# Kernel tuning notes

Hardware: AMD Instinct MI355X
Metric: run time of the kernel (lower is better)

## Reference

```python
import jax, jax.numpy as jnp
import numpy as np

N = 50000   # nodes
E = 800000  # edges (avg degree 16)
D = 128     # in_dim == hidden_dim


def setup_inputs() -> dict:
    key = jax.random.key(0)
    ks = jax.random.split(key, 8)
    x = jax.random.normal(ks[0], (N, D), dtype=jnp.float32)
    edge_index = jax.random.randint(ks[1], (2, E), 0, N, dtype=jnp.int32)
    s = 1.0 / np.sqrt(D)  # glorot-ish scale
    W0 = jax.random.normal(ks[2], (D, D), dtype=jnp.float32) * s
    W1 = jax.random.normal(ks[3], (D, D), dtype=jnp.float32) * s
    W2 = jax.random.normal(ks[4], (D, D), dtype=jnp.float32) * s
    b0 = jnp.zeros((D,), dtype=jnp.float32)
    b1 = jnp.zeros((D,), dtype=jnp.float32)
    b2 = jnp.zeros((D,), dtype=jnp.float32)
    return {"x": x, "edge_index": edge_index,
            "W0": W0, "b0": b0, "W1": W1, "b1": b1, "W2": W2, "b2": b2}


def reference(x, edge_index, W0, b0, W1, b1, W2, b2):
    # PyG GCNConv defaults: add self-loops, symmetric D^-1/2 (A+I) D^-1/2 norm,
    # linear transform first, bias added after aggregation.
    src, dst = edge_index[0], edge_index[1]
    loops = jnp.arange(N, dtype=src.dtype)
    src_f = jnp.concatenate([src, loops])  # [E+N]
    dst_f = jnp.concatenate([dst, loops])
    deg = jax.ops.segment_sum(jnp.ones_like(src_f, dtype=x.dtype), dst_f, num_segments=N)
    dinv = jnp.where(deg > 0, jax.lax.rsqrt(deg), 0.0)
    norm = dinv[src_f] * dinv[dst_f]  # [E+N]

    def gcn_layer(h, W, b):
        h = h @ W                                # [N, D]
        msg = h[src_f] * norm[:, None]           # [E+N, D] gather
        agg = jax.ops.segment_sum(msg, dst_f, num_segments=N)  # scatter-add
        return agg + b

    h = jax.nn.relu(gcn_layer(x, W0, b0))  # dropout p=0.0 is a no-op
    h = jax.nn.relu(gcn_layer(h, W1, b1))
    return gcn_layer(h, W2, b2)
```

## Files before the change

kernel.cpp:

```cpp
#include <hip/hip_runtime.h>
#include <hip/hip_fp16.h>

#define NN 50000
#define NPAD 50048
#define NE 800000
#define D 128
#define BPAD 136

typedef __attribute__((ext_vector_type(8))) short bf16x8;
typedef __attribute__((ext_vector_type(4))) float f32x4;

__device__ inline unsigned short f2bf(float f) {
    unsigned int b = __float_as_uint(f);
    return (unsigned short)((b + 0x7FFFu + ((b >> 16) & 1u)) >> 16);
}
__device__ inline float bf2f(unsigned short u) {
    return __uint_as_float(((unsigned int)u) << 16);
}


__global__ void k_degree(const int* __restrict__ dst, int* __restrict__ cnt,
                         int* __restrict__ rank) {
    int e = blockIdx.x * 256 + threadIdx.x;
    if (e < NE) {
        int d = dst[e];
        int r = atomicAdd(&cnt[d], 1);
        __builtin_nontemporal_store(r, &rank[e]);
    }
}

__global__ void k_scan_block(const int* __restrict__ cnt, int* __restrict__ excl,
                             int* __restrict__ bsum) {
    __shared__ int sm[256];
    int t = threadIdx.x;
    int idx = blockIdx.x * 256 + t;
    int v = (idx < NN) ? cnt[idx] : 0;
    sm[t] = v;
    __syncthreads();
    for (int o = 1; o < 256; o <<= 1) {
        int u = (t >= o) ? sm[t - o] : 0;
        __syncthreads();
        sm[t] += u;
        __syncthreads();
    }
    if (idx < NN) excl[idx] = sm[t] - v;
    if (t == 255) bsum[blockIdx.x] = sm[255];
}

__global__ void k_scan_top(const int* __restrict__ bsum, int* __restrict__ boff) {
    __shared__ int sm[256];
    const int NB = (NN + 255) / 256;
    int t = threadIdx.x;
    int v = (t < NB) ? bsum[t] : 0;
    sm[t] = v;
    __syncthreads();
    for (int o = 1; o < 256; o <<= 1) {
        int u = (t >= o) ? sm[t - o] : 0;
        __syncthreads();
        sm[t] += u;
        __syncthreads();
    }
    if (t < NB) boff[t] = sm[t] - v;
}

__global__ void k_scan_add(int* __restrict__ rowptr, const int* __restrict__ boff,
                           const int* __restrict__ cnt, float* __restrict__ dinv) {
    int idx = blockIdx.x * 256 + threadIdx.x;
    if (idx < NN) {
        rowptr[idx] += boff[idx >> 8];
        dinv[idx] = rsqrtf((float)(cnt[idx] + 1));
    } else if (idx == NN) {
        rowptr[NN] = NE;
    }
}

__global__ void k_fill(const int* __restrict__ src, const int* __restrict__ dst,
                       const int* __restrict__ rowptr, const int* __restrict__ rank,
                       int* __restrict__ col) {
    int e = blockIdx.x * 256 + threadIdx.x;
    if (e < NE) {
        int d = dst[e];
        int pos = rowptr[d] + rank[e];
        __builtin_nontemporal_store(src[e], &col[pos]);
    }
}


__global__ void k_convW3(const float* __restrict__ W0, const float* __restrict__ W1,
                         const float* __restrict__ W2, unsigned short* __restrict__ Wh,
                         unsigned short* __restrict__ Wl) {
    int i = blockIdx.x * 256 + threadIdx.x;
    if (i >= 3 * D * D) return;
    int m = i / (D * D), r = i - m * (D * D);
    const float* W = (m == 0) ? W0 : ((m == 1) ? W1 : W2);
    int k = r >> 7, c = r & 127;
    float v = W[r];
    unsigned short h = f2bf(v);
    unsigned short l = f2bf(v - bf2f(h));
    Wh[(size_t)m * D * D + c * D + k] = h;
    Wl[(size_t)m * D * D + c * D + k] = l;
}


__device__ inline void gemm_store(f32x4 acc[2][4], const float* __restrict__ dinv,
                                  __half* __restrict__ C, int R0, int C0, int lr, int lg) {
    #pragma unroll
    for (int fr = 0; fr < 2; fr++) {
        int rb = R0 + fr * 16 + lg * 4;
        #pragma unroll
        for (int j = 0; j < 4; j++) {
            int r = rb + j;
            if (r < NN) {
                float s = dinv[r];
                #pragma unroll
                for (int fc = 0; fc < 4; fc++)
                    C[(size_t)r * D + C0 + fc * 16 + lr] =
                        __float2half_rn(acc[fr][fc][j] * s);
            }
        }
    }
}


__global__ __launch_bounds__(256, 2) void k_gemm_mfma_x(
        const float* __restrict__ X,
        const unsigned short* __restrict__ BhT, const unsigned short* __restrict__ BlT,
        const float* __restrict__ dinv, __half* __restrict__ C) {
    __shared__ short Bs_h[D * BPAD];
    int t = threadIdx.x;
    {
        int c = t >> 1;
        int k0 = (t & 1) * 64;
        const unsigned short* gh = BhT + c * D + k0;
        short* dh = Bs_h + c * BPAD + k0;
        #pragma unroll
        for (int i = 0; i < 8; i++)
            *(int4*)(dh + i * 8) = *(const int4*)(gh + i * 8);
    }
    __syncthreads();

    int w = t >> 6, ln = t & 63;
    int wr = w >> 1, wc = w & 1;
    int R0 = blockIdx.x * 64 + wr * 32;
    int C0 = wc * 64;
    int lr = ln & 15, lg = ln >> 4;

    f32x4 acc[2][4];
    #pragma unroll
    for (int a = 0; a < 2; a++)
        #pragma unroll
        for (int b = 0; b < 4; b++)
            acc[a][b] = (f32x4){0.f, 0.f, 0.f, 0.f};

    const float* Ab = X + (size_t)(R0 + lr) * D + lg * 8;

    #pragma unroll
    for (int ks = 0; ks < 4; ks++) {
        int ko = ks * 32;
        bf16x8 fa_h[2], fa_l[2], fb_h[4], fb_l[4];
        #pragma unroll
        for (int fr = 0; fr < 2; fr++) {
            float4 p0 = *(const float4*)(Ab + fr * 16 * D + ko);
            float4 p1 = *(const float4*)(Ab + fr * 16 * D + ko + 4);
            float vv[8] = {p0.x, p0.y, p0.z, p0.w, p1.x, p1.y, p1.z, p1.w};
            #pragma unroll
            for (int j = 0; j < 8; j++) {
                unsigned short h = f2bf(vv[j]);
                fa_h[fr][j] = (short)h;
                fa_l[fr][j] = (short)f2bf(vv[j] - bf2f(h));
            }
        }
        #pragma unroll
        for (int fc = 0; fc < 4; fc++) {
            int ccol = C0 + fc * 16 + lr;
            fb_h[fc] = *(const bf16x8*)(Bs_h + ccol * BPAD + ko + lg * 8);
            fb_l[fc] = *(const bf16x8*)(BlT + (size_t)ccol * D + ko + lg * 8);
        }
        #pragma unroll
        for (int fr = 0; fr < 2; fr++) {
            #pragma unroll
            for (int fc = 0; fc < 4; fc++) {
                acc[fr][fc] = __builtin_amdgcn_mfma_f32_16x16x32_bf16(
                    fa_h[fr], fb_h[fc], acc[fr][fc], 0, 0, 0);
                acc[fr][fc] = __builtin_amdgcn_mfma_f32_16x16x32_bf16(
                    fa_l[fr], fb_h[fc], acc[fr][fc], 0, 0, 0);
                acc[fr][fc] = __builtin_amdgcn_mfma_f32_16x16x32_bf16(
                    fa_h[fr], fb_l[fc], acc[fr][fc], 0, 0, 0);
            }
        }
    }
    gemm_store(acc, dinv, C, R0, C0, lr, lg);
}


__global__ __launch_bounds__(256, 3) void k_gemm_mfma_h(
        const __half* __restrict__ H,
        const unsigned short* __restrict__ BhT, const unsigned short* __restrict__ BlT,
        const float* __restrict__ dinv, __half* __restrict__ C) {
    __shared__ short Bs_h[D * BPAD];
    int t = threadIdx.x;
    {
        int c = t >> 1;
        int k0 = (t & 1) * 64;
        const unsigned short* gh = BhT + c * D + k0;
        short* dh = Bs_h + c * BPAD + k0;
        #pragma unroll
        for (int i = 0; i < 8; i++)
            *(int4*)(dh + i * 8) = *(const int4*)(gh + i * 8);
    }
    __syncthreads();

    int w = t >> 6, ln = t & 63;
    int wr = w >> 1, wc = w & 1;
    int R0 = blockIdx.x * 64 + wr * 32;
    int C0 = wc * 64;
    int lr = ln & 15, lg = ln >> 4;

    f32x4 acc[2][4];
    #pragma unroll
    for (int a = 0; a < 2; a++)
        #pragma unroll
        for (int b = 0; b < 4; b++)
            acc[a][b] = (f32x4){0.f, 0.f, 0.f, 0.f};

    const __half* Ab = H + (size_t)(R0 + lr) * D + lg * 8;

    #pragma unroll
    for (int ks = 0; ks < 4; ks++) {
        int ko = ks * 32;
        bf16x8 fa_h[2], fa_l[2], fb_h[4], fb_l[4];
        #pragma unroll
        for (int fr = 0; fr < 2; fr++) {
            float4 p = *(const float4*)(Ab + fr * 16 * D + ko);
            const __half2* hp = (const __half2*)&p;
            #pragma unroll
            for (int q = 0; q < 4; q++) {
                float2 fv = __half22float2(hp[q]);
                unsigned short h0 = f2bf(fv.x), h1 = f2bf(fv.y);
                fa_h[fr][q * 2]     = (short)h0;
                fa_h[fr][q * 2 + 1] = (short)h1;
                fa_l[fr][q * 2]     = (short)f2bf(fv.x - bf2f(h0));
                fa_l[fr][q * 2 + 1] = (short)f2bf(fv.y - bf2f(h1));
            }
        }
        #pragma unroll
        for (int fc = 0; fc < 4; fc++) {
            int ccol = C0 + fc * 16 + lr;
            fb_h[fc] = *(const bf16x8*)(Bs_h + ccol * BPAD + ko + lg * 8);
            fb_l[fc] = *(const bf16x8*)(BlT + (size_t)ccol * D + ko + lg * 8);
        }
        #pragma unroll
        for (int fr = 0; fr < 2; fr++) {
            #pragma unroll
            for (int fc = 0; fc < 4; fc++) {
                acc[fr][fc] = __builtin_amdgcn_mfma_f32_16x16x32_bf16(
                    fa_h[fr], fb_h[fc], acc[fr][fc], 0, 0, 0);
                acc[fr][fc] = __builtin_amdgcn_mfma_f32_16x16x32_bf16(
                    fa_l[fr], fb_h[fc], acc[fr][fc], 0, 0, 0);
                acc[fr][fc] = __builtin_amdgcn_mfma_f32_16x16x32_bf16(
                    fa_h[fr], fb_l[fc], acc[fr][fc], 0, 0, 0);
            }
        }
    }
    gemm_store(acc, dinv, C, R0, C0, lr, lg);
}


__global__ __launch_bounds__(256) void k_agg_relu(const __half* __restrict__ T,
                                                  const int* __restrict__ rowptr,
                                                  const int* __restrict__ col,
                                                  const float* __restrict__ dinv,
                                                  const float* __restrict__ bias,
                                                  __half* __restrict__ Hout) {
    int i = blockIdx.x * 16 + (threadIdx.x >> 4);
    int sl = threadIdx.x & 15;
    int f = sl * 8;
    float di = dinv[i];
    float a[8];
    {
        float4 raw = *(const float4*)(T + (size_t)i * D + f);
        const __half2* hp = (const __half2*)&raw;
        #pragma unroll
        for (int q = 0; q < 4; q++) {
            float2 fv = __half22float2(hp[q]);
            a[q * 2] = fv.x;
            a[q * 2 + 1] = fv.y;
        }
    }
    int e = rowptr[i], r1 = rowptr[i + 1];
    for (; e + 8 <= r1; e += 8) {
        float4 rv[8];
        #pragma unroll
        for (int u = 0; u < 8; u++) {
            int s = col[e + u];
            rv[u] = *(const float4*)(T + (size_t)s * D + f);
        }
        #pragma unroll
        for (int u = 0; u < 8; u++) {
            const __half2* hp = (const __half2*)&rv[u];
            #pragma unroll
            for (int q = 0; q < 4; q++) {
                float2 fv = __half22float2(hp[q]);
                a[q * 2] += fv.x;
                a[q * 2 + 1] += fv.y;
            }
        }
    }
    for (; e < r1; e++) {
        int s = col[e];
        float4 rv = *(const float4*)(T + (size_t)s * D + f);
        const __half2* hp = (const __half2*)&rv;
        #pragma unroll
        for (int q = 0; q < 4; q++) {
            float2 fv = __half22float2(hp[q]);
            a[q * 2] += fv.x;
            a[q * 2 + 1] += fv.y;
        }
    }
    float4 bv0 = *(const float4*)(bias + f);
    float4 bv1 = *(const float4*)(bias + f + 4);
    float bb[8] = {bv0.x, bv0.y, bv0.z, bv0.w, bv1.x, bv1.y, bv1.z, bv1.w};
    __half2 o[4];
    #pragma unroll
    for (int q = 0; q < 4; q++) {
        float x0 = fmaxf(a[q * 2] * di + bb[q * 2], 0.f);
        float x1 = fmaxf(a[q * 2 + 1] * di + bb[q * 2 + 1], 0.f);
        o[q] = __floats2half2_rn(x0, x1);
    }
    *(float4*)(Hout + (size_t)i * D + f) = *(float4*)o;
}

__global__ __launch_bounds__(256) void k_agg_out(const __half* __restrict__ T,
                                                 const int* __restrict__ rowptr,
                                                 const int* __restrict__ col,
                                                 const float* __restrict__ dinv,
                                                 const float* __restrict__ bias,
                                                 float* __restrict__ Of) {
    int i = blockIdx.x * 16 + (threadIdx.x >> 4);
    int sl = threadIdx.x & 15;
    int f = sl * 8;
    float di = dinv[i];
    float a[8];
    {
        float4 raw = *(const float4*)(T + (size_t)i * D + f);
        const __half2* hp = (const __half2*)&raw;
        #pragma unroll
        for (int q = 0; q < 4; q++) {
            float2 fv = __half22float2(hp[q]);
            a[q * 2] = fv.x;
            a[q * 2 + 1] = fv.y;
        }
    }
    int e = rowptr[i], r1 = rowptr[i + 1];
    for (; e + 8 <= r1; e += 8) {
        float4 rv[8];
        #pragma unroll
        for (int u = 0; u < 8; u++) {
            int s = col[e + u];
            rv[u] = *(const float4*)(T + (size_t)s * D + f);
        }
        #pragma unroll
        for (int u = 0; u < 8; u++) {
            const __half2* hp = (const __half2*)&rv[u];
            #pragma unroll
            for (int q = 0; q < 4; q++) {
                float2 fv = __half22float2(hp[q]);
                a[q * 2] += fv.x;
                a[q * 2 + 1] += fv.y;
            }
        }
    }
    for (; e < r1; e++) {
        int s = col[e];
        float4 rv = *(const float4*)(T + (size_t)s * D + f);
        const __half2* hp = (const __half2*)&rv;
        #pragma unroll
        for (int q = 0; q < 4; q++) {
            float2 fv = __half22float2(hp[q]);
            a[q * 2] += fv.x;
            a[q * 2 + 1] += fv.y;
        }
    }
    float4 bv0 = *(const float4*)(bias + f);
    float4 bv1 = *(const float4*)(bias + f + 4);
    float4 o0 = make_float4(a[0] * di + bv0.x, a[1] * di + bv0.y,
                            a[2] * di + bv0.z, a[3] * di + bv0.w);
    float4 o1 = make_float4(a[4] * di + bv1.x, a[5] * di + bv1.y,
                            a[6] * di + bv1.z, a[7] * di + bv1.w);
    *(float4*)(Of + (size_t)i * D + f) = o0;
    *(float4*)(Of + (size_t)i * D + f + 4) = o1;
}


extern "C" void kernel_launch(void* const* d_in, const int* in_sizes, int n_in,
                              void* d_out, int out_size, void* d_ws, size_t ws_size,
                              hipStream_t stream) {
    const float* x  = (const float*)d_in[0];
    const int* edge = (const int*)d_in[1];
    const float* W0 = (const float*)d_in[2];
    const float* b0 = (const float*)d_in[3];
    const float* W1 = (const float*)d_in[4];
    const float* b1 = (const float*)d_in[5];
    const float* W2 = (const float*)d_in[6];
    const float* b2 = (const float*)d_in[7];
    const int* src = edge;
    const int* dst = edge + NE;
    float* out = (float*)d_out;

    char* ws = (char*)d_ws;
    size_t off = 0;
    auto alloc = [&](size_t bytes) {
        void* p = ws + off;
        off += (bytes + 255) & ~(size_t)255;
        return p;
    };
    int*   cnt    = (int*)alloc(NN * 4);
    int*   rowptr = (int*)alloc((NN + 1) * 4);
    float* dinv   = (float*)alloc(NN * 4);
    int*   bsum   = (int*)alloc(256 * 4);
    int*   boff   = (int*)alloc(256 * 4);
    int*   rank   = (int*)alloc((size_t)NE * 4);
    int*   col    = (int*)alloc((size_t)NE * 4);
    unsigned short* Wh = (unsigned short*)alloc(3 * D * D * 2);
    unsigned short* Wl = (unsigned short*)alloc(3 * D * D * 2);
    __half* Ta = (__half*)alloc((size_t)NPAD * D * 2);
    __half* Tb = (__half*)alloc((size_t)NPAD * D * 2);
    __half* Hb = (__half*)alloc((size_t)NPAD * D * 2);

    hipMemsetAsync(cnt, 0, NN * 4, stream);

    k_degree<<<(NE + 255) / 256, 256, 0, stream>>>(dst, cnt, rank);
    k_scan_block<<<(NN + 255) / 256, 256, 0, stream>>>(cnt, rowptr, bsum);
    k_scan_top<<<1, 256, 0, stream>>>(bsum, boff);
    k_scan_add<<<(NN + 256) / 256, 256, 0, stream>>>(rowptr, boff, cnt, dinv);
    k_fill<<<(NE + 255) / 256, 256, 0, stream>>>(src, dst, rowptr, rank, col);
    k_convW3<<<(3 * D * D + 255) / 256, 256, 0, stream>>>(W0, W1, W2, Wh, Wl);

    const int ggrid = (NN + 63) / 64;
    const int agrid = NN / 16;

    k_gemm_mfma_x<<<ggrid, 256, 0, stream>>>(x, Wh, Wl, dinv, Ta);
    k_agg_relu<<<agrid, 256, 0, stream>>>(Ta, rowptr, col, dinv, b0, Hb);
    k_gemm_mfma_h<<<ggrid, 256, 0, stream>>>(Hb, Wh + D * D, Wl + D * D, dinv, Tb);
    k_agg_relu<<<agrid, 256, 0, stream>>>(Tb, rowptr, col, dinv, b1, Hb);
    k_gemm_mfma_h<<<ggrid, 256, 0, stream>>>(Hb, Wh + 2 * D * D, Wl + 2 * D * D, dinv, Ta);
    k_agg_out<<<agrid, 256, 0, stream>>>(Ta, rowptr, col, dinv, b2, out);
}
```

Measured before the change: 243.6 us.

## Fuse setup kernels and load edge indices cooperatively via wave shuffles

Merges the weight bf16-split conversion into the degree-count kernel and folds the top-level scan into the block-scan kernel using a last-block ticket counter, which cuts the number of kernel launches. The aggregation kernels now load eight column indices with one coalesced load per group of lanes and broadcast them with shuffles, instead of each lane loading them all. Edges are processed in masked batches of eight with no scalar tail loop, so tail iterations issue some redundant gathers. This adds an extra memset for the counter and relies on a threadfence-based handoff between blocks.

Measured after the change: 238.5 us. 1.02x faster.

```diff
diff --git a/kernel.cpp b/kernel.cpp
--- a/kernel.cpp
+++ b/kernel.cpp
@@ -6,6 +6,8 @@
 #define NE 800000
 #define D 128
 #define BPAD 136
+#define EGRID 3125
+#define NB 196
 
 typedef __attribute__((ext_vector_type(8))) short bf16x8;
 typedef __attribute__((ext_vector_type(4))) float f32x4;
@@ -19,19 +21,39 @@
 }
 
 
-__global__ void k_degree(const int* __restrict__ dst, int* __restrict__ cnt,
-                         int* __restrict__ rank) {
-    int e = blockIdx.x * 256 + threadIdx.x;
-    if (e < NE) {
-        int d = dst[e];
-        int r = atomicAdd(&cnt[d], 1);
-        __builtin_nontemporal_store(r, &rank[e]);
+__global__ void k_degree_convW(const int* __restrict__ dst, int* __restrict__ cnt,
+                               int* __restrict__ rank,
+                               const float* __restrict__ W0, const float* __restrict__ W1,
+                               const float* __restrict__ W2,
+                               unsigned short* __restrict__ Wh, unsigned short* __restrict__ Wl) {
+    int bid = blockIdx.x;
+    int t = threadIdx.x;
+    if (bid < EGRID) {
+        int e = bid * 256 + t;
+        if (e < NE) {
+            int d = dst[e];
+            int r = atomicAdd(&cnt[d], 1);
+            __builtin_nontemporal_store(r, &rank[e]);
+        }
+    } else {
+        int i = (bid - EGRID) * 256 + t;
+        if (i >= 3 * D * D) return;
+        int m = i / (D * D), r = i - m * (D * D);
+        const float* W = (m == 0) ? W0 : ((m == 1) ? W1 : W2);
+        int k = r >> 7, c = r & 127;
+        float v = W[r];
+        unsigned short h = f2bf(v);
+        unsigned short l = f2bf(v - bf2f(h));
+        Wh[(size_t)m * D * D + c * D + k] = h;
+        Wl[(size_t)m * D * D + c * D + k] = l;
     }
 }
 
 __global__ void k_scan_block(const int* __restrict__ cnt, int* __restrict__ excl,
-                             int* __restrict__ bsum) {
+                             int* __restrict__ bsum, int* __restrict__ boff,
+                             int* __restrict__ counter) {
     __shared__ int sm[256];
+    __shared__ int lastflag;
     int t = threadIdx.x;
     int idx = blockIdx.x * 256 + t;
     int v = (idx < NN) ? cnt[idx] : 0;
@@ -45,14 +67,16 @@
     }
     if (idx < NN) excl[idx] = sm[t] - v;
     if (t == 255) bsum[blockIdx.x] = sm[255];
-}
-
-__global__ void k_scan_top(const int* __restrict__ bsum, int* __restrict__ boff) {
-    __shared__ int sm[256];
-    const int NB = (NN + 255) / 256;
-    int t = threadIdx.x;
-    int v = (t < NB) ? bsum[t] : 0;
-    sm[t] = v;
+    __threadfence();
+    if (t == 0) {
+        int ticket = atomicAdd(counter, 1);
+        lastflag = (ticket == NB - 1);
+    }
+    __syncthreads();
+    if (!lastflag) return;
+    __threadfence();
+    int v2 = (t < NB) ? bsum[t] : 0;
+    sm[t] = v2;
     __syncthreads();
     for (int o = 1; o < 256; o <<= 1) {
         int u = (t >= o) ? sm[t - o] : 0;
@@ -60,7 +84,7 @@
         sm[t] += u;
         __syncthreads();
     }
-    if (t < NB) boff[t] = sm[t] - v;
+    if (t < NB) boff[t] = sm[t] - v2;
 }
 
 __global__ void k_scan_add(int* __restrict__ rowptr, const int* __restrict__ boff,
@@ -83,22 +107,6 @@
         int pos = rowptr[d] + rank[e];
         __builtin_nontemporal_store(src[e], &col[pos]);
     }
-}
-
-
-__global__ void k_convW3(const float* __restrict__ W0, const float* __restrict__ W1,
-                         const float* __restrict__ W2, unsigned short* __restrict__ Wh,
-                         unsigned short* __restrict__ Wl) {
-    int i = blockIdx.x * 256 + threadIdx.x;
-    if (i >= 3 * D * D) return;
-    int m = i / (D * D), r = i - m * (D * D);
-    const float* W = (m == 0) ? W0 : ((m == 1) ? W1 : W2);
-    int k = r >> 7, c = r & 127;
-    float v = W[r];
-    unsigned short h = f2bf(v);
-    unsigned short l = f2bf(v - bf2f(h));
-    Wh[(size_t)m * D * D + c * D + k] = h;
-    Wl[(size_t)m * D * D + c * D + k] = l;
 }
 
 
@@ -266,6 +274,52 @@
 }
 
 
+__device__ inline void agg_accum(const float4& rv, float a[8]) {
+    const __half2* hp = (const __half2*)&rv;
+    #pragma unroll
+    for (int q = 0; q < 4; q++) {
+        float2 fv = __half22float2(hp[q]);
+        a[q * 2] += fv.x;
+        a[q * 2 + 1] += fv.y;
+    }
+}
+
+__device__ inline void agg_core(const __half* __restrict__ T,
+                                const int* __restrict__ rowptr,
+                                const int* __restrict__ col,
+                                int i, int f, int lane, float a[8]) {
+    int gb = lane & 48;
+    int sl8 = lane & 7;
+    {
+        float4 raw = *(const float4*)(T + (size_t)i * D + f);
+        const __half2* hp = (const __half2*)&raw;
+        #pragma unroll
+        for (int q = 0; q < 4; q++) {
+            float2 fv = __half22float2(hp[q]);
+            a[q * 2] = fv.x;
+            a[q * 2 + 1] = fv.y;
+        }
+    }
+    int r0 = rowptr[i], r1 = rowptr[i + 1];
+    for (int e = r0; e < r1; e += 8) {
+        int idx = e + sl8;
+        if (idx > r1 - 1) idx = r1 - 1;
+        int cv = col[idx];
+        int m = r1 - e;
+        m = m > 8 ? 8 : m;
+        int ss[8];
+        #pragma unroll
+        for (int u = 0; u < 8; u++) ss[u] = __shfl(cv, gb + u, 64);
+        float4 rv[8];
+        #pragma unroll
+        for (int u = 0; u < 8; u++)
+            rv[u] = *(const float4*)(T + (size_t)ss[u] * D + f);
+        #pragma unroll
+        for (int u = 0; u < 8; u++)
+            if (u < m) agg_accum(rv[u], a);
+    }
+}
+
 __global__ __launch_bounds__(256) void k_agg_relu(const __half* __restrict__ T,
                                                   const int* __restrict__ rowptr,
                                                   const int* __restrict__ col,
@@ -273,50 +327,12 @@
                                                   const float* __restrict__ bias,
                                                   __half* __restrict__ Hout) {
     int i = blockIdx.x * 16 + (threadIdx.x >> 4);
+    int lane = threadIdx.x & 63;
     int sl = threadIdx.x & 15;
     int f = sl * 8;
     float di = dinv[i];
     float a[8];
-    {
-        float4 raw = *(const float4*)(T + (size_t)i * D + f);
-        const __half2* hp = (const __half2*)&raw;
-        #pragma unroll
-        for (int q = 0; q < 4; q++) {
-            float2 fv = __half22float2(hp[q]);
-            a[q * 2] = fv.x;
-            a[q * 2 + 1] = fv.y;
-        }
-    }
-    int e = rowptr[i], r1 = rowptr[i + 1];
-    for (; e + 8 <= r1; e += 8) {
-        float4 rv[8];
-        #pragma unroll
-        for (int u = 0; u < 8; u++) {
-            int s = col[e + u];
-            rv[u] = *(const float4*)(T + (size_t)s * D + f);
-        }
-        #pragma unroll
-        for (int u = 0; u < 8; u++) {
-            const __half2* hp = (const __half2*)&rv[u];
-            #pragma unroll
-            for (int q = 0; q < 4; q++) {
-                float2 fv = __half22float2(hp[q]);
-                a[q * 2] += fv.x;
-                a[q * 2 + 1] += fv.y;
-            }
-        }
-    }
-    for (; e < r1; e++) {
-        int s = col[e];
-        float4 rv = *(const float4*)(T + (size_t)s * D + f);
-        const __half2* hp = (const __half2*)&rv;
-        #pragma unroll
-        for (int q = 0; q < 4; q++) {
-            float2 fv = __half22float2(hp[q]);
-            a[q * 2] += fv.x;
-            a[q * 2 + 1] += fv.y;
-        }
-    }
+    agg_core(T, rowptr, col, i, f, lane, a);
     float4 bv0 = *(const float4*)(bias + f);
     float4 bv1 = *(const float4*)(bias + f + 4);
     float bb[8] = {bv0.x, bv0.y, bv0.z, bv0.w, bv1.x, bv1.y, bv1.z, bv1.w};
@@ -337,50 +353,12 @@
                                                  const float* __restrict__ bias,
                                                  float* __restrict__ Of) {
     int i = blockIdx.x * 16 + (threadIdx.x >> 4);
+    int lane = threadIdx.x & 63;
     int sl = threadIdx.x & 15;
     int f = sl * 8;
     float di = dinv[i];
     float a[8];
-    {
-        float4 raw = *(const float4*)(T + (size_t)i * D + f);
-        const __half2* hp = (const __half2*)&raw;
-        #pragma unroll
-        for (int q = 0; q < 4; q++) {
-            float2 fv = __half22float2(hp[q]);
-            a[q * 2] = fv.x;
-            a[q * 2 + 1] = fv.y;
-        }
-    }
-    int e = rowptr[i], r1 = rowptr[i + 1];
-    for (; e + 8 <= r1; e += 8) {
-        float4 rv[8];
-        #pragma unroll
-        for (int u = 0; u < 8; u++) {
-            int s = col[e + u];
-            rv[u] = *(const float4*)(T + (size_t)s * D + f);
-        }
-        #pragma unroll
-        for (int u = 0; u < 8; u++) {
-            const __half2* hp = (const __half2*)&rv[u];
-            #pragma unroll
-            for (int q = 0; q < 4; q++) {
-                float2 fv = __half22float2(hp[q]);
-                a[q * 2] += fv.x;
-                a[q * 2 + 1] += fv.y;
-            }
-        }
-    }
-    for (; e < r1; e++) {
-        int s = col[e];
-        float4 rv = *(const float4*)(T + (size_t)s * D + f);
-        const __half2* hp = (const __half2*)&rv;
-        #pragma unroll
-        for (int q = 0; q < 4; q++) {
-            float2 fv = __half22float2(hp[q]);
-            a[q * 2] += fv.x;
-            a[q * 2 + 1] += fv.y;
-        }
-    }
+    agg_core(T, rowptr, col, i, f, lane, a);
     float4 bv0 = *(const float4*)(bias + f);
     float4 bv1 = *(const float4*)(bias + f + 4);
     float4 o0 = make_float4(a[0] * di + bv0.x, a[1] * di + bv0.y,
@@ -414,13 +392,14 @@
         off += (bytes + 255) & ~(size_t)255;
         return p;
     };
-    int*   cnt    = (int*)alloc(NN * 4);
-    int*   rowptr = (int*)alloc((NN + 1) * 4);
-    float* dinv   = (float*)alloc(NN * 4);
-    int*   bsum   = (int*)alloc(256 * 4);
-    int*   boff   = (int*)alloc(256 * 4);
-    int*   rank   = (int*)alloc((size_t)NE * 4);
-    int*   col    = (int*)alloc((size_t)NE * 4);
+    int*   cnt     = (int*)alloc(NN * 4);
+    int*   counter = (int*)alloc(256);
+    int*   rowptr  = (int*)alloc((NN + 1) * 4);
+    float* dinv    = (float*)alloc(NN * 4);
+    int*   bsum    = (int*)alloc(256 * 4);
+    int*   boff    = (int*)alloc(256 * 4);
+    int*   rank    = (int*)alloc((size_t)NE * 4);
+    int*   col     = (int*)alloc((size_t)NE * 4);
     unsigned short* Wh = (unsigned short*)alloc(3 * D * D * 2);
     unsigned short* Wl = (unsigned short*)alloc(3 * D * D * 2);
     __half* Ta = (__half*)alloc((size_t)NPAD * D * 2);
@@ -428,13 +407,12 @@
     __half* Hb = (__half*)alloc((size_t)NPAD * D * 2);
 
     hipMemsetAsync(cnt, 0, NN * 4, stream);
-
-    k_degree<<<(NE + 255) / 256, 256, 0, stream>>>(dst, cnt, rank);
-    k_scan_block<<<(NN + 255) / 256, 256, 0, stream>>>(cnt, rowptr, bsum);
-    k_scan_top<<<1, 256, 0, stream>>>(bsum, boff);
+    hipMemsetAsync(counter, 0, 256, stream);
+
+    k_degree_convW<<<EGRID + 192, 256, 0, stream>>>(dst, cnt, rank, W0, W1, W2, Wh, Wl);
+    k_scan_block<<<NB, 256, 0, stream>>>(cnt, rowptr, bsum, boff, counter);
     k_scan_add<<<(NN + 256) / 256, 256, 0, stream>>>(rowptr, boff, cnt, dinv);
-    k_fill<<<(NE + 255) / 256, 256, 0, stream>>>(src, dst, rowptr, rank, col);
-    k_convW3<<<(3 * D * D + 255) / 256, 256, 0, stream>>>(W0, W1, W2, Wh, Wl);
+    k_fill<<<EGRID, 256, 0, stream>>>(src, dst, rowptr, rank, col);
 
     const int ggrid = (NN + 63) / 64;
     const int agrid = NN / 16;
```
